# Kernel optimization log

Hardware: AMD Instinct MI355X
Metric: run time of the kernel (lower is better)

## Reference

```python
import jax, jax.numpy as jnp
import numpy as np

N_QUBITS = 12
N_LAYERS = 4
DIM = 2 ** N_QUBITS
PI = float(np.pi)


def build_design():
    # Reconstructs the gate schedule implied by the module's indexing:
    # per layer: data-encoding on each wire, Rot on each wire, CRot entangling ring.
    design = []
    for l in range(N_LAYERS):
        for q in range(N_QUBITS):
            design.append(('ENC', (q,), l))
        for q in range(N_QUBITS):
            design.append(('U3', (q,), l))
        for q in range(N_QUBITS):
            design.append(('C(U3)', (q, (q + 1) % N_QUBITS), l))
    return design

DESIGN = build_design()


def _c(a):
    return a.astype(jnp.complex64)


def mat_rx(t):
    c = _c(jnp.cos(t / 2)); s = _c(jnp.sin(t / 2))
    return jnp.stack([jnp.stack([c, -1j * s], -1), jnp.stack([-1j * s, c], -1)], -2)


def mat_ry(t):
    c = _c(jnp.cos(t / 2)); s = _c(jnp.sin(t / 2))
    return jnp.stack([jnp.stack([c, -s], -1), jnp.stack([s, c], -1)], -2)


def mat_rz(t):
    e = jnp.exp(-0.5j * _c(t)); z = jnp.zeros_like(e)
    return jnp.stack([jnp.stack([e, z], -1), jnp.stack([z, jnp.conj(e)], -1)], -2)


def mat_rot(phi, theta, omega):
    # PennyLane Rot = RZ(omega) @ RY(theta) @ RZ(phi)
    return mat_rz(omega) @ mat_ry(theta) @ mat_rz(phi)


def apply_1q(state, U, w):
    # state: (B, 2^n), wire 0 = most significant (PennyLane convention)
    B = state.shape[0]
    L = 2 ** w; R = DIM // (2 * L)
    s = state.reshape(B, L, 2, R)
    if U.ndim == 2:
        s = jnp.einsum('ij,bljr->blir', U, s)
    else:  # per-sample gate (data encoding)
        s = jnp.einsum('bij,bljr->blir', U, s)
    return s.reshape(B, DIM)


def apply_crot(state, U, c, t):
    # Apply U on target wire t for the control==1 subspace of wire c.
    B = state.shape[0]
    s = state.reshape((B,) + (2,) * N_QUBITS)
    s = jnp.moveaxis(s, (c + 1, t + 1), (1, 2)).reshape(B, 2, 2, -1)
    s1 = jnp.einsum('ij,bjr->bir', U, s[:, 1])
    s = jnp.stack([s[:, 0], s1], 1).reshape((B, 2, 2) + (2,) * (N_QUBITS - 2))
    s = jnp.moveaxis(s, (1, 2), (c + 1, t + 1))
    return s.reshape(B, DIM)


def reference(x, q_params_rot, q_params_enta):
    B = x.shape[0]
    state = jnp.zeros((B, DIM), jnp.complex64).at[:, 0].set(1.0)
    for op, wires, layer in DESIGN:
        if op == 'U3':
            q = wires[0]
            p = q_params_rot[layer, q]
            state = apply_1q(state, mat_rot(p[0], p[1], p[2]), q)
        elif op == 'C(U3)':
            cq, tq = wires
            p = q_params_enta[layer, cq]
            state = apply_crot(state, mat_rot(p[0], p[1], p[2]), cq, tq)
        else:  # data encoding: RY, RX, RZ, RY with per-sample angles
            j = wires[0]
            state = apply_1q(state, mat_ry(x[:, 0, j]), j)
            state = apply_1q(state, mat_rx(x[:, 1, j]), j)
            state = apply_1q(state, mat_rz(x[:, 2, j]), j)
            state = apply_1q(state, mat_ry(x[:, 3, j]), j)
    # <Z_i> = p(bit_i=0) - p(bit_i=1)
    probs = (jnp.abs(state) ** 2).reshape((B,) + (2,) * N_QUBITS)
    z = []
    for i in range(N_QUBITS):
        axes = tuple(a for a in range(1, N_QUBITS + 1) if a != i + 1)
        p = probs.sum(axes)
        z.append(p[:, 0] - p[:, 1])
    return jnp.stack(z, -1).astype(jnp.float32)


def setup_inputs() -> dict:
    key = jax.random.key(0)
    k1, k2, k3 = jax.random.split(key, 3)
    x = PI * jax.random.uniform(k1, (4096, 4, N_QUBITS), dtype=jnp.float32)
    q_params_rot = PI * jax.random.uniform(k2, (N_LAYERS, N_QUBITS, 3), dtype=jnp.float32)
    q_params_enta = PI * jax.random.uniform(k3, (N_LAYERS, N_QUBITS, 3), dtype=jnp.float32)
    return {'x': x, 'q_params_rot': q_params_rot, 'q_params_enta': q_params_enta}
```

## Files before the change

kernel.cpp:

```cpp
#include <hip/hip_runtime.h>
#include <math.h>

#define NQ   12
#define NL   4
#define NT   64
#define AMPS 64

typedef float cplx __attribute__((ext_vector_type(2)));

__device__ __forceinline__ cplx cpair(cplx Mx, cplx s, cplx My, cplx p) {
    cplx u;
    asm("v_pk_mul_f32 %0, %1, %2 op_sel:[0,0] op_sel_hi:[0,1]\n\t"
        "v_pk_fma_f32 %0, %1, %2, %0 op_sel:[1,1,0] op_sel_hi:[1,0,1] neg_lo:[1,0,0]\n\t"
        "v_pk_fma_f32 %0, %3, %4, %0 op_sel:[0,0,0] op_sel_hi:[0,1,1]\n\t"
        "v_pk_fma_f32 %0, %3, %4, %0 op_sel:[1,1,0] op_sel_hi:[1,0,1] neg_lo:[1,0,0]"
        : "=&v"(u) : "v"(Mx), "v"(s), "v"(My), "v"(p));
    return u;
}
__device__ __forceinline__ cplx pk_cmul(cplx a, cplx b) {
    cplx u;
    asm("v_pk_mul_f32 %0, %1, %2 op_sel:[0,0] op_sel_hi:[0,1]\n\t"
        "v_pk_fma_f32 %0, %1, %2, %0 op_sel:[1,1,0] op_sel_hi:[1,0,1] neg_lo:[1,0,0]"
        : "=&v"(u) : "v"(a), "v"(b));
    return u;
}

__device__ __forceinline__ void mm2(const cplx* A, const cplx* B, cplx* C) {
    C[0] = cpair(A[0], B[0], A[1], B[2]);
    C[1] = cpair(A[0], B[1], A[1], B[3]);
    C[2] = cpair(A[2], B[0], A[3], B[2]);
    C[3] = cpair(A[2], B[1], A[3], B[3]);
}
__device__ __forceinline__ void rotmat(float phi, float th, float om, cplx* M) {
    float ct, st_, ca, sa, cd, sd;
    sincosf(0.5f * th, &st_, &ct);
    sincosf(0.5f * (phi + om), &sa, &ca);
    sincosf(0.5f * (phi - om), &sd, &cd);
    M[0] = cplx{ct * ca, -ct * sa};
    M[1] = cplx{-st_ * cd, -st_ * sd};
    M[2] = cplx{st_ * cd, -st_ * sd};
    M[3] = cplx{ct * ca, ct * sa};
}
__device__ __forceinline__ void rowsel(const cplx* M, bool hi, cplx& Mx, cplx& My) {
    Mx = hi ? M[3] : M[0];
    My = hi ? M[2] : M[1];
}

template<int CTRL>
__device__ __forceinline__ float dpp_perm(float v) {
    return __int_as_float(__builtin_amdgcn_update_dpp(
        __float_as_int(v), __float_as_int(v), CTRL, 0xF, 0xF, false));
}
template<int XM>
__device__ __forceinline__ float partner(float v) {
    if constexpr (XM == 8)      return dpp_perm<0x128>(v);
    else if constexpr (XM == 2) return dpp_perm<0x4E>(v);
    else if constexpr (XM == 1) return dpp_perm<0xB1>(v);
    else                        return __shfl_xor(v, XM, 64);
}

template<int XM>
__device__ __forceinline__ void lane_gate(cplx* s, cplx Mx, cplx My) {
    #pragma unroll
    for (int j0 = 0; j0 < AMPS; j0 += 4) {
        cplx pv[4];
        #pragma unroll
        for (int j = 0; j < 4; ++j) {
            pv[j].x = partner<XM>(s[j0 + j].x);
            pv[j].y = partner<XM>(s[j0 + j].y);
        }
        #pragma unroll
        for (int j = 0; j < 4; ++j)
            s[j0 + j] = cpair(Mx, s[j0 + j], My, pv[j]);
    }
}
template<int K>
__device__ __forceinline__ void local_gate(cplx* s, cplx M0, cplx M1, cplx M2, cplx M3) {
    #pragma unroll
    for (int j = 0; j < AMPS; ++j) {
        if ((j >> K) & 1) continue;
        const int i1 = j | (1 << K);
        cplx v0 = s[j], v1 = s[i1];
        s[j]  = cpair(M0, v0, M1, v1);
        s[i1] = cpair(M2, v0, M3, v1);
    }
}
template<int CB, int TB>
__device__ __forceinline__ void cgate_local(cplx* s, const cplx* A, const cplx* B) {
    cplx A0 = A[0], A1 = A[1], A2 = A[2], A3 = A[3];
    cplx B0 = B[0], B1 = B[1], B2 = B[2], B3 = B[3];
    #pragma unroll
    for (int j = 0; j < AMPS; ++j) {
        if ((j >> TB) & 1) continue;
        const int i1 = j | (1 << TB);
        cplx v0 = s[j], v1 = s[i1];
        if ((j >> CB) & 1) {
            s[j]  = cpair(B0, v0, B1, v1);
            s[i1] = cpair(B2, v0, B3, v1);
        } else {
            s[j]  = cpair(A0, v0, A1, v1);
            s[i1] = cpair(A2, v0, A3, v1);
        }
    }
}

__global__ __launch_bounds__(NT, 1) void qsim_kernel(
    const float* __restrict__ x,
    const float* __restrict__ prot,
    const float* __restrict__ penta,
    float* __restrict__ out)
{
    __shared__ cplx xbuf[640];
    __shared__ cplx GA[NL * NQ][4];
    __shared__ cplx GB[NL * NQ][4];
    __shared__ cplx ltab[AMPS];

    cplx* ENCp = xbuf;
    cplx* RMp  = xbuf + 48;
    cplx* EMp  = xbuf + 240;
    cplx* UUp  = xbuf + 432;

    const int tid = threadIdx.x;
    const int b   = blockIdx.x;

    if (tid < NQ) {
        const int q = tid;
        const float* xb = x + (size_t)b * 4 * NQ;
        const float t0 = xb[q], t1 = xb[NQ + q], t2 = xb[2 * NQ + q], t3 = xb[3 * NQ + q];
        float c, s;
        sincosf(0.5f * t0, &s, &c);
        cplx R0[4] = {cplx{c, 0.f}, cplx{-s, 0.f}, cplx{s, 0.f}, cplx{c, 0.f}};
        sincosf(0.5f * t1, &s, &c);
        cplx R1[4] = {cplx{c, 0.f}, cplx{0.f, -s}, cplx{0.f, -s}, cplx{c, 0.f}};
        sincosf(0.5f * t2, &s, &c);
        cplx R2[4] = {cplx{c, -s}, cplx{0.f, 0.f}, cplx{0.f, 0.f}, cplx{c, s}};
        sincosf(0.5f * t3, &s, &c);
        cplx R3[4] = {cplx{c, 0.f}, cplx{-s, 0.f}, cplx{s, 0.f}, cplx{c, 0.f}};
        cplx T1[4], T2[4], E[4];
        mm2(R1, R0, T1);
        mm2(R2, T1, T2);
        mm2(R3, T2, E);
        #pragma unroll
        for (int i = 0; i < 4; ++i) ENCp[q * 4 + i] = E[i];
    }
    if (tid < NL * NQ) {
        cplx M[4];
        rotmat(prot[3 * tid], prot[3 * tid + 1], prot[3 * tid + 2], M);
        #pragma unroll
        for (int i = 0; i < 4; ++i) RMp[tid * 4 + i] = M[i];
        rotmat(penta[3 * tid], penta[3 * tid + 1], penta[3 * tid + 2], M);
        #pragma unroll
        for (int i = 0; i < 4; ++i) EMp[tid * 4 + i] = M[i];
    }
    __syncthreads();
    if (tid < NL * NQ) {
        cplx U[4];
        mm2(RMp + tid * 4, ENCp + (tid % NQ) * 4, U);
        #pragma unroll
        for (int i = 0; i < 4; ++i) UUp[tid * 4 + i] = U[i];
    }
    __syncthreads();
    if (tid < NL * NQ) {
        const int l = tid / NQ, q = tid - l * NQ;
        cplx A[4], B[4];
        if (q < 11) {
            if (l == 0) { A[0] = cplx{1.f,0.f}; A[1] = cplx{0.f,0.f}; A[2] = cplx{0.f,0.f}; A[3] = cplx{1.f,0.f}; }
            else {
                #pragma unroll
                for (int i = 0; i < 4; ++i) A[i] = UUp[(l * NQ + q + 1) * 4 + i];
            }
            mm2(EMp + tid * 4, A, B);
        } else {
            if (l == NL - 1) { A[0] = cplx{1.f,0.f}; A[1] = cplx{0.f,0.f}; A[2] = cplx{0.f,0.f}; A[3] = cplx{1.f,0.f}; }
            else {
                #pragma unroll
                for (int i = 0; i < 4; ++i) A[i] = UUp[((l + 1) * NQ) * 4 + i];
            }
            mm2(A, EMp + tid * 4, B);
        }
        #pragma unroll
        for (int i = 0; i < 4; ++i) { GA[tid][i] = A[i]; GB[tid][i] = B[i]; }
    }
    {
        cplx m = cplx{1.f, 0.f};
        #pragma unroll
        for (int wq = 6; wq < 12; ++wq) {
            const int bit = (tid >> (11 - wq)) & 1;
            m = pk_cmul(m, bit ? UUp[wq * 4 + 2] : UUp[wq * 4 + 0]);
        }
        ltab[tid] = m;
    }
    cplx lp = cplx{1.f, 0.f};
    #pragma unroll
    for (int wq = 0; wq < 6; ++wq) {
        const int bit = (tid >> (5 - wq)) & 1;
        lp = pk_cmul(lp, bit ? UUp[wq * 4 + 2] : UUp[wq * 4 + 0]);
    }
    __syncthreads();

    cplx s[AMPS];
    #pragma unroll
    for (int j = 0; j < AMPS; ++j) s[j] = pk_cmul(lp, ltab[j]);

    for (int l = 0; l < NL; ++l) {
        const int g = l * NQ;
        {
            const cplx* M = (tid & 32) ? &GB[g + 0][0] : &GA[g + 0][0];
            cplx Mx, My; rowsel(M, tid & 16, Mx, My);
            lane_gate<16>(s, Mx, My);
        }
        {
            const cplx* M = (tid & 16) ? &GB[g + 1][0] : &GA[g + 1][0];
            cplx Mx, My; rowsel(M, tid & 8, Mx, My);
            lane_gate<8>(s, Mx, My);
        }
        {
            const cplx* M = (tid & 8) ? &GB[g + 2][0] : &GA[g + 2][0];
            cplx Mx, My; rowsel(M, tid & 4, Mx, My);
            lane_gate<4>(s, Mx, My);
        }
        {
            const cplx* M = (tid & 4) ? &GB[g + 3][0] : &GA[g + 3][0];
            cplx Mx, My; rowsel(M, tid & 2, Mx, My);
            lane_gate<2>(s, Mx, My);
        }
        {
            const cplx* M = (tid & 2) ? &GB[g + 4][0] : &GA[g + 4][0];
            cplx Mx, My; rowsel(M, tid & 1, Mx, My);
            lane_gate<1>(s, Mx, My);
        }
        {
            const cplx* M = (tid & 1) ? &GB[g + 5][0] : &GA[g + 5][0];
            local_gate<5>(s, M[0], M[1], M[2], M[3]);
        }
        cgate_local<5, 4>(s, &GA[g + 6][0], &GB[g + 6][0]);
        cgate_local<4, 3>(s, &GA[g + 7][0], &GB[g + 7][0]);
        cgate_local<3, 2>(s, &GA[g + 8][0], &GB[g + 8][0]);
        cgate_local<2, 1>(s, &GA[g + 9][0], &GB[g + 9][0]);
        cgate_local<1, 0>(s, &GA[g + 10][0], &GB[g + 10][0]);
        {
            cplx Ax, Ay, Bx, By;
            rowsel(&GA[g + 11][0], tid & 32, Ax, Ay);
            rowsel(&GB[g + 11][0], tid & 32, Bx, By);
            #pragma unroll
            for (int j0 = 0; j0 < AMPS; j0 += 4) {
                cplx pv[4];
                #pragma unroll
                for (int j = 0; j < 4; ++j) {
                    pv[j].x = __shfl_xor(s[j0 + j].x, 32, 64);
                    pv[j].y = __shfl_xor(s[j0 + j].y, 32, 64);
                }
                #pragma unroll
                for (int j = 0; j < 4; ++j) {
                    if ((j0 + j) & 1) s[j0 + j] = cpair(Bx, s[j0 + j], By, pv[j]);
                    else              s[j0 + j] = cpair(Ax, s[j0 + j], Ay, pv[j]);
                }
            }
        }
    }

    float psum = 0.f;
    float zl[6] = {0.f, 0.f, 0.f, 0.f, 0.f, 0.f};
    #pragma unroll
    for (int j = 0; j < AMPS; ++j) {
        cplx v = s[j];
        float pr = fmaf(v.x, v.x, v.y * v.y);
        psum += pr;
        int pb = __float_as_int(pr);
        #pragma unroll
        for (int i = 0; i < 6; ++i)
            zl[i] += __int_as_float(pb ^ (((j >> (5 - i)) & 1) << 31));
    }
    float zv[NQ];
    #pragma unroll
    for (int i = 0; i < 6; ++i)
        zv[i] = ((tid >> (5 - i)) & 1) ? -psum : psum;
    #pragma unroll
    for (int i = 0; i < 6; ++i) zv[6 + i] = zl[i];
    #pragma unroll
    for (int q = 0; q < NQ; ++q) {
        float v = zv[q];
        #pragma unroll
        for (int off = 32; off > 0; off >>= 1) v += __shfl_xor(v, off, 64);
        zv[q] = v;
    }
    if (tid == 0) {
        float* ob = out + (size_t)b * NQ;
        #pragma unroll
        for (int q = 0; q < NQ; ++q) ob[q] = zv[q];
    }
}

extern "C" void kernel_launch(void* const* d_in, const int* in_sizes, int n_in,
                              void* d_out, int out_size, void* d_ws, size_t ws_size,
                              hipStream_t stream) {
    const float* x     = (const float*)d_in[0];
    const float* prot  = (const float*)d_in[1];
    const float* penta = (const float*)d_in[2];
    float* out = (float*)d_out;
    const int B = in_sizes[0] / (4 * NQ);
    qsim_kernel<<<B, NT, 0, stream>>>(x, prot, penta, out);
}
```

Measured before the change: 157.4 us.

## Fold first layer's entangling gates into the factorized product-state initialization

```diff
diff --git a/kernel.cpp b/kernel.cpp
--- a/kernel.cpp
+++ b/kernel.cpp
@@ -57,6 +57,13 @@
     else if constexpr (XM == 2) return dpp_perm<0x4E>(v);
     else if constexpr (XM == 1) return dpp_perm<0xB1>(v);
     else                        return __shfl_xor(v, XM, 64);
+}
+template<int XM>
+__device__ __forceinline__ cplx partner_c(cplx v) {
+    cplx p;
+    p.x = partner<XM>(v.x);
+    p.y = partner<XM>(v.y);
+    return p;
 }
 
 template<int XM>
@@ -104,6 +111,21 @@
     }
 }
 
+template<int XM>
+__device__ __forceinline__ cplx pref_gate(cplx lp, const cplx* Bm, bool cbit, bool tbit) {
+    cplx Mx, My; rowsel(Bm, tbit, Mx, My);
+    cplx p = partner_c<XM>(lp);
+    cplx nl = cpair(Mx, lp, My, p);
+    return cbit ? nl : lp;
+}
+template<int XM>
+__device__ __forceinline__ cplx tab_gate(cplx t, const cplx* Bm, bool cbit, bool tbit) {
+    cplx Mx, My; rowsel(Bm, tbit, Mx, My);
+    cplx p = partner_c<XM>(t);
+    cplx nt = cpair(Mx, t, My, p);
+    return cbit ? nt : t;
+}
+
 __global__ __launch_bounds__(NT, 1) void qsim_kernel(
     const float* __restrict__ x,
     const float* __restrict__ prot,
@@ -113,7 +135,7 @@
     __shared__ cplx xbuf[640];
     __shared__ cplx GA[NL * NQ][4];
     __shared__ cplx GB[NL * NQ][4];
-    __shared__ cplx ltab[AMPS];
+    __shared__ cplx ltab2[2][AMPS];
 
     cplx* ENCp = xbuf;
     cplx* RMp  = xbuf + 48;
@@ -181,14 +203,13 @@
         #pragma unroll
         for (int i = 0; i < 4; ++i) { GA[tid][i] = A[i]; GB[tid][i] = B[i]; }
     }
-    {
-        cplx m = cplx{1.f, 0.f};
-        #pragma unroll
-        for (int wq = 6; wq < 12; ++wq) {
-            const int bit = (tid >> (11 - wq)) & 1;
-            m = pk_cmul(m, bit ? UUp[wq * 4 + 2] : UUp[wq * 4 + 0]);
-        }
-        ltab[tid] = m;
+    __syncthreads();
+
+    cplx t0 = cplx{1.f, 0.f};
+    #pragma unroll
+    for (int wq = 6; wq < 12; ++wq) {
+        const int bit = (tid >> (11 - wq)) & 1;
+        t0 = pk_cmul(t0, bit ? UUp[wq * 4 + 2] : UUp[wq * 4 + 0]);
     }
     cplx lp = cplx{1.f, 0.f};
     #pragma unroll
@@ -196,13 +217,46 @@
         const int bit = (tid >> (5 - wq)) & 1;
         lp = pk_cmul(lp, bit ? UUp[wq * 4 + 2] : UUp[wq * 4 + 0]);
     }
+    lp = pref_gate<16>(lp, &GB[0][0], tid & 32, tid & 16);
+    lp = pref_gate<8 >(lp, &GB[1][0], tid & 16, tid & 8);
+    lp = pref_gate<4 >(lp, &GB[2][0], tid & 8,  tid & 4);
+    lp = pref_gate<2 >(lp, &GB[3][0], tid & 4,  tid & 2);
+    lp = pref_gate<1 >(lp, &GB[4][0], tid & 2,  tid & 1);
+    cplx tB;
+    {
+        cplx Mx, My; rowsel(&GB[5][0], tid & 32, Mx, My);
+        tB = cpair(Mx, t0, My, partner_c<32>(t0));
+    }
+    t0 = tab_gate<16>(t0, &GB[6][0],  tid & 32, tid & 16);
+    tB = tab_gate<16>(tB, &GB[6][0],  tid & 32, tid & 16);
+    t0 = tab_gate<8 >(t0, &GB[7][0],  tid & 16, tid & 8);
+    tB = tab_gate<8 >(tB, &GB[7][0],  tid & 16, tid & 8);
+    t0 = tab_gate<4 >(t0, &GB[8][0],  tid & 8,  tid & 4);
+    tB = tab_gate<4 >(tB, &GB[8][0],  tid & 8,  tid & 4);
+    t0 = tab_gate<2 >(t0, &GB[9][0],  tid & 4,  tid & 2);
+    tB = tab_gate<2 >(tB, &GB[9][0],  tid & 4,  tid & 2);
+    t0 = tab_gate<1 >(t0, &GB[10][0], tid & 2,  tid & 1);
+    tB = tab_gate<1 >(tB, &GB[10][0], tid & 2,  tid & 1);
+    cplx lpA, lpB;
+    {
+        cplx p = partner_c<32>(lp);
+        cplx Mx, My;
+        rowsel(&GA[11][0], tid & 32, Mx, My);
+        lpA = cpair(Mx, lp, My, p);
+        rowsel(&GB[11][0], tid & 32, Mx, My);
+        lpB = cpair(Mx, lp, My, p);
+    }
+    ltab2[0][tid] = t0;
+    ltab2[1][tid] = tB;
     __syncthreads();
 
+    const cplx* T = ltab2[tid & 1];
     cplx s[AMPS];
     #pragma unroll
-    for (int j = 0; j < AMPS; ++j) s[j] = pk_cmul(lp, ltab[j]);
-
-    for (int l = 0; l < NL; ++l) {
+    for (int j = 0; j < AMPS; ++j)
+        s[j] = pk_cmul((j & 1) ? lpB : lpA, T[j]);
+
+    for (int l = 1; l < NL; ++l) {
         const int g = l * NQ;
         {
             const cplx* M = (tid & 32) ? &GB[g + 0][0] : &GA[g + 0][0];
```

Result: faster. 126.7 us (-19.5%).
